# Kernel optimization log

Hardware: AMD Instinct MI355X
Metric: run time of the kernel (lower is better)

## Reference

```python
import jax, jax.numpy as jnp
import numpy as np

DIM = 384
HEADS = 12
WS = 7
N = WS * WS * WS  # 343
B = 128
TABLE = (2 * WS - 1) ** 3  # 2197


def _relative_position_index(ws):
    coords = np.stack(np.meshgrid(np.arange(ws), np.arange(ws), np.arange(ws), indexing='ij'))
    cf = coords.reshape(3, -1)  # (3, N)
    rel = cf[:, :, None] - cf[:, None, :]  # (3, N, N)
    rel = rel.transpose(1, 2, 0) + (ws - 1)  # (N, N, 3), shifted to >=0
    rel[:, :, 0] *= (2 * ws - 1) * (2 * ws - 1)
    rel[:, :, 1] *= (2 * ws - 1)
    return rel.sum(-1).astype(np.int32)  # (N, N)


def setup_inputs() -> dict:
    key = jax.random.key(0)
    ks = jax.random.split(key, 6)
    x = jax.random.normal(ks[0], (B, N, DIM), dtype=jnp.float32)
    qkv_w = jax.random.normal(ks[1], (3 * DIM, DIM), dtype=jnp.float32) * (DIM ** -0.5)
    qkv_b = jnp.zeros((3 * DIM,), dtype=jnp.float32)
    proj_w = jax.random.normal(ks[2], (DIM, DIM), dtype=jnp.float32) * (DIM ** -0.5)
    proj_b = jnp.zeros((DIM,), dtype=jnp.float32)
    bias_table = jax.random.normal(ks[3], (TABLE, HEADS), dtype=jnp.float32) * 0.02
    rel_index = jnp.asarray(_relative_position_index(WS))
    return {"x": x, "qkv_w": qkv_w, "qkv_b": qkv_b, "proj_w": proj_w,
            "proj_b": proj_b, "bias_table": bias_table, "rel_index": rel_index}


def reference(x, qkv_w, qkv_b, proj_w, proj_b, bias_table, rel_index):
    Bn, Nn, C = x.shape
    hd = C // HEADS
    scale = hd ** -0.5
    qkv = x @ qkv_w.T + qkv_b  # (B, N, 3C)
    qkv = qkv.reshape(Bn, Nn, 3, HEADS, hd)
    q, k, v = jnp.moveaxis(qkv, 2, 0)  # each (B, N, H, hd)
    q = jnp.swapaxes(q, 1, 2) * scale  # (B, H, N, hd)
    k = jnp.swapaxes(k, 1, 2)
    v = jnp.swapaxes(v, 1, 2)
    attn = jnp.einsum('bhnd,bhmd->bhnm', q, k)  # (B, H, N, N)
    bias = bias_table[rel_index]  # (N, N, H) gathered per pair
    attn = attn + jnp.transpose(bias, (2, 0, 1))[None]  # (B, H, N, N)
    attn = jax.nn.softmax(attn, axis=-1)
    out = jnp.einsum('bhnm,bhmd->bhnd', attn, v)  # (B, H, N, hd)
    out = jnp.swapaxes(out, 1, 2).reshape(Bn, Nn, C)
    return out @ proj_w.T + proj_b
```

## Files before the change

### kernel.cpp

```cpp
#include <hip/hip_runtime.h>

typedef _Float16 f16;
typedef _Float16 half8 __attribute__((ext_vector_type(8)));
typedef _Float16 half4 __attribute__((ext_vector_type(4)));
typedef float f32x4 __attribute__((ext_vector_type(4)));

#define NTOK 343
#define NHEADS 12
#define NBATCH 128
#define HD 32
#define KDIM 384
#define QKV_LD 1152
#define BIAS_LD 384

static __device__ __forceinline__ void gload16(const f16* g, f16* l) {
  __builtin_amdgcn_global_load_lds((const __attribute__((address_space(1))) void*)g,
                                   (__attribute__((address_space(3))) void*)l, 16, 0, 0);
}

__global__ __launch_bounds__(256) void cvt_f32_f16(const float* __restrict__ src,
                                                   f16* __restrict__ dst, int n4) {
  int stride = gridDim.x * blockDim.x;
  for (int i = blockIdx.x * blockDim.x + threadIdx.x; i < n4; i += stride) {
    float4 v = reinterpret_cast<const float4*>(src)[i];
    half4 h;
    h[0] = (f16)v.x; h[1] = (f16)v.y; h[2] = (f16)v.z; h[3] = (f16)v.w;
    reinterpret_cast<half4*>(dst)[i] = h;
  }
}

__global__ __launch_bounds__(384) void bias_expand(const float* __restrict__ table,
                                                   const int* __restrict__ rel,
                                                   f16* __restrict__ out) {
  int q = blockIdx.x, h = blockIdx.y, kv = threadIdx.x;
  int kvc = kv < NTOK ? kv : NTOK - 1;
  int idx = rel[q * NTOK + kvc];
  f16 v = (kv < NTOK) ? (f16)table[idx * NHEADS + h] : (f16)0.f;
  out[((size_t)h * NTOK + q) * BIAS_LD + kv] = v;
}

__device__ __forceinline__ void gemm128_body(const f16* __restrict__ A,
                                             const f16* __restrict__ Bw,
                                             int mtile, int ntile,
                                             f32x4 acc[4][4],
                                             f16* As, f16* Bs) {
  const int tid = threadIdx.x;
  const int lane = tid & 63;
  const int w = tid >> 6;
  const int wm = w >> 1, wn = w & 1;

  #pragma unroll
  for (int i = 0; i < 4; ++i)
    #pragma unroll
    for (int j = 0; j < 4; ++j) { f32x4 z = {0.f,0.f,0.f,0.f}; acc[i][j] = z; }

  const int lrow = w * 8 + (lane >> 3);
  const int lcol = (lane & 7) * 8;
  const f16* Ab = A + (size_t)(mtile*128 + lrow) * KDIM + lcol;
  const f16* Bb = Bw + (size_t)(ntile*128 + lrow) * KDIM + lcol;

  for (int k0 = 0; k0 < KDIM; k0 += 64) {
    __syncthreads();
    #pragma unroll
    for (int rnd = 0; rnd < 4; ++rnd) {
      gload16(Ab + (size_t)rnd*32*KDIM + k0, As + rnd*2048 + w*512);
      gload16(Bb + (size_t)rnd*32*KDIM + k0, Bs + rnd*2048 + w*512);
    }
    __syncthreads();
    #pragma unroll
    for (int kk = 0; kk < 2; ++kk) {
      half8 af[4], bf[4];
      #pragma unroll
      for (int mi = 0; mi < 4; ++mi)
        af[mi] = *reinterpret_cast<half8*>(&As[(wm*64 + mi*16 + (lane & 15))*64 + kk*32 + (lane >> 4)*8]);
      #pragma unroll
      for (int ni = 0; ni < 4; ++ni)
        bf[ni] = *reinterpret_cast<half8*>(&Bs[(wn*64 + ni*16 + (lane & 15))*64 + kk*32 + (lane >> 4)*8]);
      #pragma unroll
      for (int mi = 0; mi < 4; ++mi)
        #pragma unroll
        for (int ni = 0; ni < 4; ++ni)
          acc[mi][ni] = __builtin_amdgcn_mfma_f32_16x16x32_f16(af[mi], bf[ni], acc[mi][ni], 0, 0, 0);
    }
  }
}

__global__ __launch_bounds__(256) void qkv_gemm(const f16* __restrict__ xb,
                                                const f16* __restrict__ wq,
                                                const float* __restrict__ qkv_b,
                                                f16* __restrict__ qkvb) {
  __shared__ __align__(16) f16 smem[17408];
  f16* As = smem;
  f16* Bs = smem + 8192;
  const int ntile = blockIdx.x, mtile = blockIdx.y;
  f32x4 acc[4][4];
  gemm128_body(xb, wq, mtile, ntile, acc, As, Bs);

  const int tid = threadIdx.x;
  const int lane = tid & 63;
  const int w = tid >> 6;
  const int wm = w >> 1, wn = w & 1;
  const float scale = (ntile < 3) ? 0.17677669529663687f : 1.0f;

  float bj[4];
  #pragma unroll
  for (int ni = 0; ni < 4; ++ni)
    bj[ni] = qkv_b[ntile*128 + wn*64 + ni*16 + (lane & 15)];

  __syncthreads();
  f16* Cs = smem;
  #pragma unroll
  for (int ni = 0; ni < 4; ++ni) {
    int col = wn*64 + ni*16 + (lane & 15);
    #pragma unroll
    for (int mi = 0; mi < 4; ++mi)
      #pragma unroll
      for (int r = 0; r < 4; ++r) {
        int row = wm*64 + mi*16 + (lane >> 4)*4 + r;
        Cs[row*136 + col] = (f16)((acc[mi][ni][r] + bj[ni]) * scale);
      }
  }
  __syncthreads();
  #pragma unroll
  for (int p = 0; p < 8; ++p) {
    int row = p*16 + (tid >> 4);
    int col = (tid & 15) * 8;
    float4 v = *reinterpret_cast<float4*>(&Cs[row*136 + col]);
    *reinterpret_cast<float4*>(&qkvb[(size_t)(mtile*128 + row)*QKV_LD + ntile*128 + col]) = v;
  }
}

__global__ __launch_bounds__(256) void vtrans(const f16* __restrict__ qkvb,
                                              f16* __restrict__ vt) {
  __shared__ __align__(16) f16 T[64][40];
  const int tid = threadIdx.x;
  const int nt = blockIdx.x, h = blockIdx.y, b = blockIdx.z;
  {
    int row = tid >> 2, ch = tid & 3;
    int n = nt*64 + row; int nc = n < NTOK ? n : NTOK - 1;
    *reinterpret_cast<float4*>(&T[row][ch*8]) =
        *reinterpret_cast<const float4*>(&qkvb[((size_t)b*NTOK + nc)*QKV_LD + 2*KDIM + h*HD + ch*8]);
  }
  __syncthreads();
  int d = tid >> 3, c2 = tid & 7;
  half8 o;
  #pragma unroll
  for (int e = 0; e < 8; ++e) o[e] = T[c2*8 + e][d];
  *reinterpret_cast<half8*>(&vt[((size_t)(b*NHEADS + h)*HD + d)*KDIM + nt*64 + c2*8]) = o;
}

__global__ __launch_bounds__(256) void attn_kernel(const f16* __restrict__ qkvb,
                                                   const f16* __restrict__ vt,
                                                   const f16* __restrict__ bfp,
                                                   f16* __restrict__ ab) {
  __shared__ __align__(16) f16 Qs[64][40];
  __shared__ __align__(16) f16 Ks[64][40];
  __shared__ __align__(16) f16 Vs[32][72];
  __shared__ __align__(16) f16 Ps[64][72];
  __shared__ __align__(16) f16 Bb[64][72];
  const int tid = threadIdx.x;
  const int lane = tid & 63;
  const int wave = tid >> 6;
  const int qt = blockIdx.x;
  const int h = blockIdx.y;
  const int b = blockIdx.z;
  const size_t bh = (size_t)b * NHEADS + h;

  {
    int row = tid >> 2, ch = tid & 3;
    int n = qt*64 + row; int nc = n < NTOK ? n : NTOK - 1;
    *reinterpret_cast<float4*>(&Qs[row][ch*8]) =
        *reinterpret_cast<const float4*>(&qkvb[((size_t)b*NTOK + nc)*QKV_LD + h*HD + ch*8]);
  }
  __syncthreads();
  half8 aq = *reinterpret_cast<half8*>(&Qs[wave*16 + (lane & 15)][(lane >> 4)*8]);

  float m_run[4], l_run[4];
  f32x4 o0 = {0.f,0.f,0.f,0.f}, o1 = {0.f,0.f,0.f,0.f};
  #pragma unroll
  for (int r = 0; r < 4; ++r) { m_run[r] = -3.0e38f; l_run[r] = 0.f; }

  for (int kvt = 0; kvt < 6; ++kvt) {
    {
      int row = tid >> 2, ch = tid & 3;
      int kv = kvt*64 + row; int n = kv < NTOK ? kv : NTOK - 1;
      *reinterpret_cast<float4*>(&Ks[row][ch*8]) =
          *reinterpret_cast<const float4*>(&qkvb[((size_t)b*NTOK + n)*QKV_LD + KDIM + h*HD + ch*8]);
      int d = tid >> 3, c2 = tid & 7;
      *reinterpret_cast<float4*>(&Vs[d][c2*8]) =
          *reinterpret_cast<const float4*>(&vt[(bh*HD + d)*KDIM + kvt*64 + c2*8]);
      #pragma unroll
      for (int i = 0; i < 2; ++i) {
        int brow = (tid >> 3) + i*32;
        int q = qt*64 + brow; int qc = q < NTOK ? q : NTOK - 1;
        *reinterpret_cast<float4*>(&Bb[brow][c2*8]) =
            *reinterpret_cast<const float4*>(&bfp[((size_t)h*NTOK + qc)*BIAS_LD + kvt*64 + c2*8]);
      }
    }
    __syncthreads();

    f32x4 s[4];
    #pragma unroll
    for (int nt = 0; nt < 4; ++nt) {
      half8 bk = *reinterpret_cast<half8*>(&Ks[nt*16 + (lane & 15)][(lane >> 4)*8]);
      f32x4 z = {0.f,0.f,0.f,0.f};
      s[nt] = __builtin_amdgcn_mfma_f32_16x16x32_f16(aq, bk, z, 0, 0, 0);
    }

    float sv[4][4]; float rmax[4];
    #pragma unroll
    for (int r = 0; r < 4; ++r) rmax[r] = -3.0e38f;
    #pragma unroll
    for (int nt = 0; nt < 4; ++nt) {
      int kv = kvt*64 + nt*16 + (lane & 15);
      bool kvok = kv < NTOK;
      #pragma unroll
      for (int r = 0; r < 4; ++r) {
        int ql = wave*16 + (lane >> 4)*4 + r;
        float x = s[nt][r] + (float)Bb[ql][nt*16 + (lane & 15)];
        x = kvok ? x : -1.0e30f;
        sv[nt][r] = x;
        rmax[r] = fmaxf(rmax[r], x);
      }
    }
    #pragma unroll
    for (int r = 0; r < 4; ++r) {
      float v = rmax[r];
      v = fmaxf(v, __shfl_xor(v, 1));
      v = fmaxf(v, __shfl_xor(v, 2));
      v = fmaxf(v, __shfl_xor(v, 4));
      v = fmaxf(v, __shfl_xor(v, 8));
      rmax[r] = v;
    }
    #pragma unroll
    for (int r = 0; r < 4; ++r) {
      float mnew = fmaxf(m_run[r], rmax[r]);
      float sf = __expf(m_run[r] - mnew);
      m_run[r] = mnew;
      l_run[r] *= sf;
      o0[r] *= sf; o1[r] *= sf;
      float rs = 0.f;
      int qrow = wave*16 + (lane >> 4)*4 + r;
      #pragma unroll
      for (int nt = 0; nt < 4; ++nt) {
        float p = __expf(sv[nt][r] - mnew);
        rs += p;
        Ps[qrow][nt*16 + (lane & 15)] = (f16)p;
      }
      rs += __shfl_xor(rs, 1);
      rs += __shfl_xor(rs, 2);
      rs += __shfl_xor(rs, 4);
      rs += __shfl_xor(rs, 8);
      l_run[r] += rs;
    }

    half8 ap0 = *reinterpret_cast<half8*>(&Ps[wave*16 + (lane & 15)][(lane >> 4)*8]);
    half8 ap1 = *reinterpret_cast<half8*>(&Ps[wave*16 + (lane & 15)][32 + (lane >> 4)*8]);
    half8 bv;
    bv = *reinterpret_cast<half8*>(&Vs[(lane & 15)][(lane >> 4)*8]);
    o0 = __builtin_amdgcn_mfma_f32_16x16x32_f16(ap0, bv, o0, 0, 0, 0);
    bv = *reinterpret_cast<half8*>(&Vs[(lane & 15)][32 + (lane >> 4)*8]);
    o0 = __builtin_amdgcn_mfma_f32_16x16x32_f16(ap1, bv, o0, 0, 0, 0);
    bv = *reinterpret_cast<half8*>(&Vs[16 + (lane & 15)][(lane >> 4)*8]);
    o1 = __builtin_amdgcn_mfma_f32_16x16x32_f16(ap0, bv, o1, 0, 0, 0);
    bv = *reinterpret_cast<half8*>(&Vs[16 + (lane & 15)][32 + (lane >> 4)*8]);
    o1 = __builtin_amdgcn_mfma_f32_16x16x32_f16(ap1, bv, o1, 0, 0, 0);
    __syncthreads();
  }

  #pragma unroll
  for (int r = 0; r < 4; ++r) {
    int qrow = wave*16 + (lane >> 4)*4 + r;
    float inv = 1.f / l_run[r];
    Ps[qrow][(lane & 15)]      = (f16)(o0[r] * inv);
    Ps[qrow][16 + (lane & 15)] = (f16)(o1[r] * inv);
  }
  {
    int row = tid >> 2, ch = tid & 3;
    int q = qt*64 + row;
    if (q < NTOK) {
      float4 v = *reinterpret_cast<float4*>(&Ps[row][ch*8]);
      *reinterpret_cast<float4*>(&ab[((size_t)b*NTOK + q)*KDIM + h*HD + ch*8]) = v;
    }
  }
}

__global__ __launch_bounds__(256) void proj_gemm(const f16* __restrict__ ab,
                                                 const f16* __restrict__ wp,
                                                 const float* __restrict__ proj_b,
                                                 float* __restrict__ out) {
  __shared__ __align__(16) f16 smem[16384];
  f16* As = smem;
  f16* Bs = smem + 8192;
  const int ntile = blockIdx.x, mtile = blockIdx.y;
  f32x4 acc[4][4];
  gemm128_body(ab, wp, mtile, ntile, acc, As, Bs);
  const int lane = threadIdx.x & 63;
  const int w = threadIdx.x >> 6;
  const int wm = w >> 1, wn = w & 1;
  #pragma unroll
  for (int ni = 0; ni < 4; ++ni) {
    int j = ntile*128 + wn*64 + ni*16 + (lane & 15);
    float pb = proj_b[j];
    #pragma unroll
    for (int mi = 0; mi < 4; ++mi)
      #pragma unroll
      for (int r = 0; r < 4; ++r) {
        int m = mtile*128 + wm*64 + mi*16 + (lane >> 4)*4 + r;
        out[(size_t)m*KDIM + j] = acc[mi][ni][r] + pb;
      }
  }
}

extern "C" void kernel_launch(void* const* d_in, const int* in_sizes, int n_in,
                              void* d_out, int out_size, void* d_ws, size_t ws_size,
                              hipStream_t stream) {
  const float* x          = (const float*)d_in[0];
  const float* qkv_w      = (const float*)d_in[1];
  const float* qkv_b      = (const float*)d_in[2];
  const float* proj_w     = (const float*)d_in[3];
  const float* proj_b     = (const float*)d_in[4];
  const float* bias_table = (const float*)d_in[5];
  const int*   rel_index  = (const int*)d_in[6];

  const size_t M = (size_t)NBATCH * NTOK;
  char* p = (char*)d_ws;
  auto alloc = [&](size_t bytes) { void* r = (void*)p; p += (bytes + 255) & ~(size_t)255; return r; };
  f16* xb   = (f16*)alloc(M * KDIM * 2);
  f16* wq   = (f16*)alloc((size_t)3 * KDIM * KDIM * 2);
  f16* wp   = (f16*)alloc((size_t)KDIM * KDIM * 2);
  f16* qkvb = (f16*)alloc(M * QKV_LD * 2);
  f16* vt   = (f16*)alloc((size_t)NBATCH*NHEADS*HD*KDIM*2);
  f16* bfp  = (f16*)alloc((size_t)NHEADS*NTOK*BIAS_LD*2);
  f16* ab   = xb;

  cvt_f32_f16<<<4096, 256, 0, stream>>>(x, xb, (int)(M * KDIM / 4));
  cvt_f32_f16<<<432, 256, 0, stream>>>(qkv_w, wq, 3 * KDIM * KDIM / 4);
  cvt_f32_f16<<<144, 256, 0, stream>>>(proj_w, wp, KDIM * KDIM / 4);
  bias_expand<<<dim3(NTOK, NHEADS), 384, 0, stream>>>(bias_table, rel_index, bfp);
  qkv_gemm<<<dim3(9, 343), 256, 0, stream>>>(xb, wq, qkv_b, qkvb);
  vtrans<<<dim3(6, NHEADS, NBATCH), 256, 0, stream>>>(qkvb, vt);
  attn_kernel<<<dim3(6, NHEADS, NBATCH), 256, 0, stream>>>(qkvb, vt, bfp, ab);
  proj_gemm<<<dim3(3, 343), 256, 0, stream>>>(ab, wp, proj_b, (float*)d_out);
}
```

Before: 444.3 us.

## Restructure attention kernel: transposed S, register prefetch, permuted bias, exp2, XCD remap

Rewrites the attention inner loop to compute S transposed (K as the A operand), so each lane owns one query row and the softmax reductions shrink to two cross-lane shuffles. K, V and bias tiles for the next kv tile are prefetched into registers while the current tile is computed. The bias is precomputed in an MFMA-fragment-permuted layout with LOG2E folded in and masking baked in as -30000, and the softmax uses exp2. The Q scale also absorbs LOG2E. Workgroup IDs in the qkv, attention and projection kernels are remapped so tiles are grouped per XCD for L2 locality. The cost is more register pressure and a more complex index layout.

```diff
diff --git a/kernel.cpp b/kernel.cpp
--- a/kernel.cpp
+++ b/kernel.cpp
@@ -3,6 +3,7 @@
 typedef _Float16 f16;
 typedef _Float16 half8 __attribute__((ext_vector_type(8)));
 typedef _Float16 half4 __attribute__((ext_vector_type(4)));
+typedef __fp16 fp16x2 __attribute__((ext_vector_type(2)));
 typedef float f32x4 __attribute__((ext_vector_type(4)));
 
 #define NTOK 343
@@ -11,7 +12,7 @@
 #define HD 32
 #define KDIM 384
 #define QKV_LD 1152
-#define BIAS_LD 384
+#define LOG2E 1.4426950408889634f
 
 static __device__ __forceinline__ void gload16(const f16* g, f16* l) {
   __builtin_amdgcn_global_load_lds((const __attribute__((address_space(1))) void*)g,
@@ -29,14 +30,25 @@
   }
 }
 
-__global__ __launch_bounds__(384) void bias_expand(const float* __restrict__ table,
-                                                   const int* __restrict__ rel,
-                                                   f16* __restrict__ out) {
-  int q = blockIdx.x, h = blockIdx.y, kv = threadIdx.x;
-  int kvc = kv < NTOK ? kv : NTOK - 1;
-  int idx = rel[q * NTOK + kvc];
-  f16 v = (kv < NTOK) ? (f16)table[idx * NHEADS + h] : (f16)0.f;
-  out[((size_t)h * NTOK + q) * BIAS_LD + kv] = v;
+__global__ __launch_bounds__(256) void bperm_gen(const float* __restrict__ table,
+                                                 const int* __restrict__ rel,
+                                                 f16* __restrict__ out) {
+  const int qt = blockIdx.x / 6, kvt = blockIdx.x % 6, h = blockIdx.y;
+  const int wave = threadIdx.x >> 6, lane = threadIdx.x & 63;
+  const int qi = lane & 15, G = lane >> 4;
+  int q = qt*64 + wave*16 + qi; int qc = q < NTOK ? q : NTOK - 1;
+  f16 vals[16];
+  #pragma unroll
+  for (int nt = 0; nt < 4; ++nt)
+    #pragma unroll
+    for (int r = 0; r < 4; ++r) {
+      int kv = kvt*64 + nt*16 + G*4 + r;
+      float v = (kv < NTOK) ? table[rel[qc*NTOK + kv]*NHEADS + h] * LOG2E : -30000.0f;
+      vals[nt*4+r] = (f16)v;
+    }
+  f16* dst = out + ((((size_t)h*6 + qt)*6 + kvt)*4 + wave)*1024 + lane*16;
+  *reinterpret_cast<half8*>(dst)     = *reinterpret_cast<half8*>(&vals[0]);
+  *reinterpret_cast<half8*>(dst + 8) = *reinterpret_cast<half8*>(&vals[8]);
 }
 
 __device__ __forceinline__ void gemm128_body(const f16* __restrict__ A,
@@ -92,7 +104,11 @@
   __shared__ __align__(16) f16 smem[17408];
   f16* As = smem;
   f16* Bs = smem + 8192;
-  const int ntile = blockIdx.x, mtile = blockIdx.y;
+  int orig = blockIdx.x + 9*blockIdx.y;
+  int xcd = orig & 7, off = orig >> 3;
+  int wg = (xcd < 7 ? xcd*386 : 2702 + (xcd-7)*385) + off;
+  const int ntile = wg % 9, mtile = wg / 9;
+
   f32x4 acc[4][4];
   gemm128_body(xb, wq, mtile, ntile, acc, As, Bs);
 
@@ -100,7 +116,7 @@
   const int lane = tid & 63;
   const int w = tid >> 6;
   const int wm = w >> 1, wn = w & 1;
-  const float scale = (ntile < 3) ? 0.17677669529663687f : 1.0f;
+  const float scale = (ntile < 3) ? 0.17677669529663687f * LOG2E : 1.0f;
 
   float bj[4];
   #pragma unroll
@@ -151,135 +167,149 @@
 
 __global__ __launch_bounds__(256) void attn_kernel(const f16* __restrict__ qkvb,
                                                    const f16* __restrict__ vt,
-                                                   const f16* __restrict__ bfp,
+                                                   const f16* __restrict__ bperm,
                                                    f16* __restrict__ ab) {
   __shared__ __align__(16) f16 Qs[64][40];
   __shared__ __align__(16) f16 Ks[64][40];
   __shared__ __align__(16) f16 Vs[32][72];
-  __shared__ __align__(16) f16 Ps[64][72];
-  __shared__ __align__(16) f16 Bb[64][72];
+  __shared__ __align__(16) f16 PB[4][2][4][144];
   const int tid = threadIdx.x;
   const int lane = tid & 63;
   const int wave = tid >> 6;
-  const int qt = blockIdx.x;
-  const int h = blockIdx.y;
-  const int b = blockIdx.z;
+  const int qi = lane & 15;
+  const int G = lane >> 4;
+  int orig = blockIdx.x + 6*blockIdx.y + 72*blockIdx.z;
+  int wg = (orig & 7) * 1152 + (orig >> 3);
+  const int qt = wg % 6;
+  const int h  = (wg / 6) % 12;
+  const int b  = wg / 72;
   const size_t bh = (size_t)b * NHEADS + h;
 
   {
     int row = tid >> 2, ch = tid & 3;
-    int n = qt*64 + row; int nc = n < NTOK ? n : NTOK - 1;
+    int n = qt*64 + row; n = n < NTOK ? n : NTOK - 1;
     *reinterpret_cast<float4*>(&Qs[row][ch*8]) =
-        *reinterpret_cast<const float4*>(&qkvb[((size_t)b*NTOK + nc)*QKV_LD + h*HD + ch*8]);
+        *reinterpret_cast<const float4*>(&qkvb[((size_t)b*NTOK + n)*QKV_LD + h*HD + ch*8]);
   }
   __syncthreads();
-  half8 aq = *reinterpret_cast<half8*>(&Qs[wave*16 + (lane & 15)][(lane >> 4)*8]);
-
-  float m_run[4], l_run[4];
+  half8 aq = *reinterpret_cast<half8*>(&Qs[wave*16 + qi][G*8]);
+
+  const f16* bp = bperm + ((((size_t)h*6 + qt)*6)*4 + wave)*1024 + lane*16;
+
+  const int krow = tid >> 2, kch = tid & 3;
+  const int vd = tid >> 3, vch = tid & 7;
+  float4 kreg, vreg; half8 bb0, bb1;
+  {
+    int n = krow; n = n < NTOK ? n : NTOK - 1;
+    kreg = *reinterpret_cast<const float4*>(&qkvb[((size_t)b*NTOK + n)*QKV_LD + KDIM + h*HD + kch*8]);
+    vreg = *reinterpret_cast<const float4*>(&vt[(bh*HD + vd)*KDIM + vch*8]);
+    bb0 = *reinterpret_cast<const half8*>(bp);
+    bb1 = *reinterpret_cast<const half8*>(bp + 8);
+  }
+
+  float m_run = -3.0e38f, l_run = 0.f;
   f32x4 o0 = {0.f,0.f,0.f,0.f}, o1 = {0.f,0.f,0.f,0.f};
-  #pragma unroll
-  for (int r = 0; r < 4; ++r) { m_run[r] = -3.0e38f; l_run[r] = 0.f; }
 
   for (int kvt = 0; kvt < 6; ++kvt) {
-    {
-      int row = tid >> 2, ch = tid & 3;
-      int kv = kvt*64 + row; int n = kv < NTOK ? kv : NTOK - 1;
-      *reinterpret_cast<float4*>(&Ks[row][ch*8]) =
-          *reinterpret_cast<const float4*>(&qkvb[((size_t)b*NTOK + n)*QKV_LD + KDIM + h*HD + ch*8]);
-      int d = tid >> 3, c2 = tid & 7;
-      *reinterpret_cast<float4*>(&Vs[d][c2*8]) =
-          *reinterpret_cast<const float4*>(&vt[(bh*HD + d)*KDIM + kvt*64 + c2*8]);
-      #pragma unroll
-      for (int i = 0; i < 2; ++i) {
-        int brow = (tid >> 3) + i*32;
-        int q = qt*64 + brow; int qc = q < NTOK ? q : NTOK - 1;
-        *reinterpret_cast<float4*>(&Bb[brow][c2*8]) =
-            *reinterpret_cast<const float4*>(&bfp[((size_t)h*NTOK + qc)*BIAS_LD + kvt*64 + c2*8]);
+    __syncthreads();
+    *reinterpret_cast<float4*>(&Ks[krow][kch*8]) = kreg;
+    *reinterpret_cast<float4*>(&Vs[vd][vch*8]) = vreg;
+    half8 cb0 = bb0, cb1 = bb1;
+    if (kvt < 5) {
+      int n = (kvt+1)*64 + krow; n = n < NTOK ? n : NTOK - 1;
+      kreg = *reinterpret_cast<const float4*>(&qkvb[((size_t)b*NTOK + n)*QKV_LD + KDIM + h*HD + kch*8]);
+      vreg = *reinterpret_cast<const float4*>(&vt[(bh*HD + vd)*KDIM + (kvt+1)*64 + vch*8]);
+      bb0 = *reinterpret_cast<const half8*>(bp + (kvt+1)*4096);
+      bb1 = *reinterpret_cast<const half8*>(bp + (kvt+1)*4096 + 8);
+    }
+    __syncthreads();
+
+    f32x4 s[4];
+    half8 ak0 = *reinterpret_cast<half8*>(&Ks[ 0 + qi][G*8]);
+    half8 ak1 = *reinterpret_cast<half8*>(&Ks[16 + qi][G*8]);
+    half8 ak2 = *reinterpret_cast<half8*>(&Ks[32 + qi][G*8]);
+    half8 ak3 = *reinterpret_cast<half8*>(&Ks[48 + qi][G*8]);
+    f32x4 z = {0.f,0.f,0.f,0.f};
+    __builtin_amdgcn_s_setprio(1);
+    s[0] = __builtin_amdgcn_mfma_f32_16x16x32_f16(ak0, aq, z, 0, 0, 0);
+    s[1] = __builtin_amdgcn_mfma_f32_16x16x32_f16(ak1, aq, z, 0, 0, 0);
+    s[2] = __builtin_amdgcn_mfma_f32_16x16x32_f16(ak2, aq, z, 0, 0, 0);
+    s[3] = __builtin_amdgcn_mfma_f32_16x16x32_f16(ak3, aq, z, 0, 0, 0);
+    __builtin_amdgcn_s_setprio(0);
+
+    #pragma unroll
+    for (int nt = 0; nt < 4; ++nt)
+      #pragma unroll
+      for (int r = 0; r < 4; ++r)
+        s[nt][r] += (float)((nt < 2) ? cb0[nt*4+r] : cb1[(nt-2)*4+r]);
+
+    float mx0 = fmaxf(fmaxf(s[0][0], s[0][1]), fmaxf(s[0][2], s[0][3]));
+    float mx1 = fmaxf(fmaxf(s[1][0], s[1][1]), fmaxf(s[1][2], s[1][3]));
+    float mx2 = fmaxf(fmaxf(s[2][0], s[2][1]), fmaxf(s[2][2], s[2][3]));
+    float mx3 = fmaxf(fmaxf(s[3][0], s[3][1]), fmaxf(s[3][2], s[3][3]));
+    float mx = fmaxf(fmaxf(mx0, mx1), fmaxf(mx2, mx3));
+    mx = fmaxf(mx, __shfl_xor(mx, 16));
+    mx = fmaxf(mx, __shfl_xor(mx, 32));
+
+    float mnew = fmaxf(m_run, mx);
+    float corr = exp2f(m_run - mnew);
+    m_run = mnew;
+    l_run *= corr;
+    #pragma unroll
+    for (int r = 0; r < 4; ++r) { o0[r] *= corr; o1[r] *= corr; }
+
+    float ts = 0.f;
+    #pragma unroll
+    for (int nt = 0; nt < 4; ++nt)
+      #pragma unroll
+      for (int r = 0; r < 4; ++r) {
+        float pv = exp2f(s[nt][r] - mnew);
+        s[nt][r] = pv;
+        ts += pv;
       }
-    }
-    __syncthreads();
-
-    f32x4 s[4];
+    ts += __shfl_xor(ts, 16);
+    ts += __shfl_xor(ts, 32);
+    l_run += ts;
+
     #pragma unroll
     for (int nt = 0; nt < 4; ++nt) {
-      half8 bk = *reinterpret_cast<half8*>(&Ks[nt*16 + (lane & 15)][(lane >> 4)*8]);
-      f32x4 z = {0.f,0.f,0.f,0.f};
-      s[nt] = __builtin_amdgcn_mfma_f32_16x16x32_f16(aq, bk, z, 0, 0, 0);
-    }
-
-    float sv[4][4]; float rmax[4];
-    #pragma unroll
-    for (int r = 0; r < 4; ++r) rmax[r] = -3.0e38f;
-    #pragma unroll
-    for (int nt = 0; nt < 4; ++nt) {
-      int kv = kvt*64 + nt*16 + (lane & 15);
-      bool kvok = kv < NTOK;
-      #pragma unroll
-      for (int r = 0; r < 4; ++r) {
-        int ql = wave*16 + (lane >> 4)*4 + r;
-        float x = s[nt][r] + (float)Bb[ql][nt*16 + (lane & 15)];
-        x = kvok ? x : -1.0e30f;
-        sv[nt][r] = x;
-        rmax[r] = fmaxf(rmax[r], x);
+      int Gt = 2*(nt & 1) + (G >> 1);
+      int sN = nt >> 1;
+      #pragma unroll
+      for (int rr = 0; rr < 2; ++rr) {
+        fp16x2 ph = __builtin_amdgcn_cvt_pkrtz(s[nt][2*rr], s[nt][2*rr+1]);
+        int eb = (G & 1)*4 + 2*rr;
+        *reinterpret_cast<fp16x2*>(&PB[wave][sN][Gt][qi*8 + eb]) = ph;
       }
     }
-    #pragma unroll
-    for (int r = 0; r < 4; ++r) {
-      float v = rmax[r];
-      v = fmaxf(v, __shfl_xor(v, 1));
-      v = fmaxf(v, __shfl_xor(v, 2));
-      v = fmaxf(v, __shfl_xor(v, 4));
-      v = fmaxf(v, __shfl_xor(v, 8));
-      rmax[r] = v;
-    }
-    #pragma unroll
-    for (int r = 0; r < 4; ++r) {
-      float mnew = fmaxf(m_run[r], rmax[r]);
-      float sf = __expf(m_run[r] - mnew);
-      m_run[r] = mnew;
-      l_run[r] *= sf;
-      o0[r] *= sf; o1[r] *= sf;
-      float rs = 0.f;
-      int qrow = wave*16 + (lane >> 4)*4 + r;
-      #pragma unroll
-      for (int nt = 0; nt < 4; ++nt) {
-        float p = __expf(sv[nt][r] - mnew);
-        rs += p;
-        Ps[qrow][nt*16 + (lane & 15)] = (f16)p;
-      }
-      rs += __shfl_xor(rs, 1);
-      rs += __shfl_xor(rs, 2);
-      rs += __shfl_xor(rs, 4);
-      rs += __shfl_xor(rs, 8);
-      l_run[r] += rs;
-    }
-
-    half8 ap0 = *reinterpret_cast<half8*>(&Ps[wave*16 + (lane & 15)][(lane >> 4)*8]);
-    half8 ap1 = *reinterpret_cast<half8*>(&Ps[wave*16 + (lane & 15)][32 + (lane >> 4)*8]);
-    half8 bv;
-    bv = *reinterpret_cast<half8*>(&Vs[(lane & 15)][(lane >> 4)*8]);
-    o0 = __builtin_amdgcn_mfma_f32_16x16x32_f16(ap0, bv, o0, 0, 0, 0);
-    bv = *reinterpret_cast<half8*>(&Vs[(lane & 15)][32 + (lane >> 4)*8]);
-    o0 = __builtin_amdgcn_mfma_f32_16x16x32_f16(ap1, bv, o0, 0, 0, 0);
-    bv = *reinterpret_cast<half8*>(&Vs[16 + (lane & 15)][(lane >> 4)*8]);
-    o1 = __builtin_amdgcn_mfma_f32_16x16x32_f16(ap0, bv, o1, 0, 0, 0);
-    bv = *reinterpret_cast<half8*>(&Vs[16 + (lane & 15)][32 + (lane >> 4)*8]);
-    o1 = __builtin_amdgcn_mfma_f32_16x16x32_f16(ap1, bv, o1, 0, 0, 0);
-    __syncthreads();
-  }
-
-  #pragma unroll
-  for (int r = 0; r < 4; ++r) {
-    int qrow = wave*16 + (lane >> 4)*4 + r;
-    float inv = 1.f / l_run[r];
-    Ps[qrow][(lane & 15)]      = (f16)(o0[r] * inv);
-    Ps[qrow][16 + (lane & 15)] = (f16)(o1[r] * inv);
+
+    half8 pb0 = *reinterpret_cast<half8*>(&PB[wave][0][G][qi*8]);
+    half8 pb1 = *reinterpret_cast<half8*>(&PB[wave][1][G][qi*8]);
+    half8 av00 = *reinterpret_cast<half8*>(&Vs[qi][G*8]);
+    half8 av01 = *reinterpret_cast<half8*>(&Vs[qi][32 + G*8]);
+    half8 av10 = *reinterpret_cast<half8*>(&Vs[16 + qi][G*8]);
+    half8 av11 = *reinterpret_cast<half8*>(&Vs[16 + qi][32 + G*8]);
+    __builtin_amdgcn_s_setprio(1);
+    o0 = __builtin_amdgcn_mfma_f32_16x16x32_f16(av00, pb0, o0, 0, 0, 0);
+    o0 = __builtin_amdgcn_mfma_f32_16x16x32_f16(av01, pb1, o0, 0, 0, 0);
+    o1 = __builtin_amdgcn_mfma_f32_16x16x32_f16(av10, pb0, o1, 0, 0, 0);
+    o1 = __builtin_amdgcn_mfma_f32_16x16x32_f16(av11, pb1, o1, 0, 0, 0);
+    __builtin_amdgcn_s_setprio(0);
+  }
+
+  float inv = 1.f / l_run;
+  #pragma unroll
+  for (int rr = 0; rr < 2; ++rr) {
+    fp16x2 a = __builtin_amdgcn_cvt_pkrtz(o0[2*rr]*inv, o0[2*rr+1]*inv);
+    *reinterpret_cast<fp16x2*>(&Qs[wave*16 + qi][G*4 + 2*rr]) = a;
+    fp16x2 c = __builtin_amdgcn_cvt_pkrtz(o1[2*rr]*inv, o1[2*rr+1]*inv);
+    *reinterpret_cast<fp16x2*>(&Qs[wave*16 + qi][16 + G*4 + 2*rr]) = c;
   }
   {
-    int row = tid >> 2, ch = tid & 3;
-    int q = qt*64 + row;
+    int row = lane >> 2, ch = lane & 3;
+    int q = qt*64 + wave*16 + row;
     if (q < NTOK) {
-      float4 v = *reinterpret_cast<float4*>(&Ps[row][ch*8]);
+      float4 v = *reinterpret_cast<float4*>(&Qs[wave*16 + row][ch*8]);
       *reinterpret_cast<float4*>(&ab[((size_t)b*NTOK + q)*KDIM + h*HD + ch*8]) = v;
     }
   }
@@ -292,7 +322,11 @@
   __shared__ __align__(16) f16 smem[16384];
   f16* As = smem;
   f16* Bs = smem + 8192;
-  const int ntile = blockIdx.x, mtile = blockIdx.y;
+  int orig = blockIdx.x + 3*blockIdx.y;
+  int xcd = orig & 7, off = orig >> 3;
+  int wg = (xcd < 5 ? xcd*129 : 645 + (xcd-5)*128) + off;
+  const int ntile = wg % 3, mtile = wg / 3;
+
   f32x4 acc[4][4];
   gemm128_body(ab, wp, mtile, ntile, acc, As, Bs);
   const int lane = threadIdx.x & 63;
@@ -326,20 +360,20 @@
   const size_t M = (size_t)NBATCH * NTOK;
   char* p = (char*)d_ws;
   auto alloc = [&](size_t bytes) { void* r = (void*)p; p += (bytes + 255) & ~(size_t)255; return r; };
-  f16* xb   = (f16*)alloc(M * KDIM * 2);
-  f16* wq   = (f16*)alloc((size_t)3 * KDIM * KDIM * 2);
-  f16* wp   = (f16*)alloc((size_t)KDIM * KDIM * 2);
-  f16* qkvb = (f16*)alloc(M * QKV_LD * 2);
-  f16* vt   = (f16*)alloc((size_t)NBATCH*NHEADS*HD*KDIM*2);
-  f16* bfp  = (f16*)alloc((size_t)NHEADS*NTOK*BIAS_LD*2);
-  f16* ab   = xb;
+  f16* xb    = (f16*)alloc(M * KDIM * 2);
+  f16* wq    = (f16*)alloc((size_t)3 * KDIM * KDIM * 2);
+  f16* wp    = (f16*)alloc((size_t)KDIM * KDIM * 2);
+  f16* qkvb  = (f16*)alloc(M * QKV_LD * 2);
+  f16* vt    = (f16*)alloc((size_t)NBATCH*NHEADS*HD*KDIM*2);
+  f16* bperm = (f16*)alloc((size_t)NHEADS*6*6*4*64*16*2);
+  f16* ab    = xb;
 
   cvt_f32_f16<<<4096, 256, 0, stream>>>(x, xb, (int)(M * KDIM / 4));
   cvt_f32_f16<<<432, 256, 0, stream>>>(qkv_w, wq, 3 * KDIM * KDIM / 4);
   cvt_f32_f16<<<144, 256, 0, stream>>>(proj_w, wp, KDIM * KDIM / 4);
-  bias_expand<<<dim3(NTOK, NHEADS), 384, 0, stream>>>(bias_table, rel_index, bfp);
+  bperm_gen<<<dim3(36, NHEADS), 256, 0, stream>>>(bias_table, rel_index, bperm);
   qkv_gemm<<<dim3(9, 343), 256, 0, stream>>>(xb, wq, qkv_b, qkvb);
   vtrans<<<dim3(6, NHEADS, NBATCH), 256, 0, stream>>>(qkvb, vt);
-  attn_kernel<<<dim3(6, NHEADS, NBATCH), 256, 0, stream>>>(qkvb, vt, bfp, ab);
+  attn_kernel<<<dim3(6, NHEADS, NBATCH), 256, 0, stream>>>(qkvb, vt, bperm, ab);
   proj_gemm<<<dim3(3, 343), 256, 0, stream>>>(ab, wp, proj_b, (float*)d_out);
 }
```

New measurement: 366.8 us. 17.4% less time.
